# Kernel tuning notes

Measured on AMD Instinct MI355X. Metric: run time of the kernel, lower is better.

The kernel has to match this reference:

```python
import jax, jax.numpy as jnp
import numpy as np

B, S, IN = 32, 512, 19
DE, DD = 256, 128      # encoder / decoder d_model
HE, HD = 8, 4          # heads
LE, LD = 6, 2          # layers
FE, FD = 4 * DE, 4 * DD
EPS = 1e-5


def _ln(x, g, b):
    m = x.mean(-1, keepdims=True)
    v = ((x - m) ** 2).mean(-1, keepdims=True)
    return (x - m) / jnp.sqrt(v + EPS) * g + b


def _mha(x, qkv_w, qkv_b, out_w, out_b, kpad, nh):
    Bq, Sq, D = x.shape
    dh = D // nh
    qkv = x @ qkv_w.T + qkv_b
    q, k, v = jnp.split(qkv, 3, axis=-1)
    hs = lambda t: t.reshape(Bq, Sq, nh, dh).transpose(0, 2, 1, 3)  # -> [B,h,S,dh]
    q, k, v = hs(q), hs(k), hs(v)
    scores = jnp.einsum('bhqd,bhkd->bhqk', q, k) / float(np.sqrt(dh))
    scores = jnp.where(kpad[:, None, None, :], -1e9, scores)  # mask padded keys
    attn = jax.nn.softmax(scores, axis=-1)
    o = jnp.einsum('bhqk,bhkd->bhqd', attn, v).transpose(0, 2, 1, 3).reshape(Bq, Sq, D)
    return o @ out_w.T + out_b


def _block(x, p, kpad, nh):
    qkv_w, qkv_b, ow, ob, f1w, f1b, f2w, f2b, g1, b1, g2, b2 = p
    x = _ln(x + _mha(x, qkv_w, qkv_b, ow, ob, kpad, nh), g1, b1)
    h = jax.nn.relu(x @ f1w.T + f1b) @ f2w.T + f2b
    return _ln(x + h, g2, b2)


def _run(x, ps, kpad, nh, L):
    for i in range(L):
        x = _block(x, tuple(p[i] for p in ps), kpad, nh)
    return x


def _forward(event_tensor, w_in_enc, b_in_enc,
             enc_qkv_w, enc_qkv_b, enc_out_w, enc_out_b,
             enc_f1_w, enc_f1_b, enc_f2_w, enc_f2_b,
             enc_g1, enc_b1, enc_g2, enc_b2,
             mask_token, e2d_w,
             dec_qkv_w, dec_qkv_b, dec_out_w, dec_out_b,
             dec_f1_w, dec_f1_b, dec_f2_w, dec_f2_b,
             dec_g1, dec_b1, dec_g2, dec_b2,
             qh_w, qh_b, dth_w, dth_b,
             attention_mask, pred_mask):
    visible = attention_mask & (~pred_mask)
    counts = visible.sum(axis=1)                                  # [B]
    order = jnp.argsort(~visible, axis=1, stable=True)            # visible positions packed first, in order
    tok = event_tensor @ w_in_enc.T + b_in_enc                    # [B,S,DE]
    vis = jnp.take_along_axis(tok, order[:, :, None], axis=1)
    pos = jnp.arange(S)
    enc_pad = pos[None, :] >= counts[:, None]                      # True = padded slot
    vis = jnp.where(enc_pad[:, :, None], 0.0, vis)
    enc_ps = (enc_qkv_w, enc_qkv_b, enc_out_w, enc_out_b, enc_f1_w, enc_f1_b,
              enc_f2_w, enc_f2_b, enc_g1, enc_b1, enc_g2, enc_b2)
    enc_out = _run(vis, enc_ps, enc_pad, HE, LE)
    dec_vis = enc_out @ e2d_w.T                                    # [B,S,DD]
    idx = jnp.cumsum(visible.astype(jnp.int32), axis=1) - 1        # position -> packed index
    gathered = jnp.take_along_axis(dec_vis, jnp.clip(idx, 0)[:, :, None], axis=1)
    dec_in = jnp.where(visible[:, :, None], gathered, mask_token)  # mask token at masked/pad slots
    dec_ps = (dec_qkv_w, dec_qkv_b, dec_out_w, dec_out_b, dec_f1_w, dec_f1_b,
              dec_f2_w, dec_f2_b, dec_g1, dec_b1, dec_g2, dec_b2)
    dec_out = _run(dec_in, dec_ps, ~attention_mask, HD, LD)
    q = dec_out @ qh_w.T + qh_b
    dt = dec_out @ dth_w.T + dth_b
    return jnp.concatenate([q, dt], axis=-1)                       # [B,S,2]


def setup_inputs():
    key = jax.random.key(0)
    ks = iter(jax.random.split(key, 64))
    nrm = lambda shp, s=0.02: jax.random.normal(next(ks), shp, jnp.float32) * s
    d = {}
    d['event_tensor'] = jax.random.normal(next(ks), (B, S, IN), jnp.float32)
    lengths = jax.random.randint(next(ks), (B,), S // 2, S + 1)
    pos = jnp.arange(S)
    am = pos[None, :] < lengths[:, None]
    pm = (jax.random.uniform(next(ks), (B, S)) < 0.75) & am
    pm = pm.at[:, 0].set(False)  # guarantee >=1 visible token per row
    d['attention_mask'] = am
    d['pred_mask'] = pm
    d['w_in_enc'] = nrm((DE, IN)); d['b_in_enc'] = jnp.zeros((DE,), jnp.float32)
    d['enc_qkv_w'] = nrm((LE, 3 * DE, DE)); d['enc_qkv_b'] = jnp.zeros((LE, 3 * DE), jnp.float32)
    d['enc_out_w'] = nrm((LE, DE, DE));     d['enc_out_b'] = jnp.zeros((LE, DE), jnp.float32)
    d['enc_f1_w'] = nrm((LE, FE, DE));      d['enc_f1_b'] = jnp.zeros((LE, FE), jnp.float32)
    d['enc_f2_w'] = nrm((LE, DE, FE));      d['enc_f2_b'] = jnp.zeros((LE, DE), jnp.float32)
    d['enc_g1'] = jnp.ones((LE, DE), jnp.float32); d['enc_b1'] = jnp.zeros((LE, DE), jnp.float32)
    d['enc_g2'] = jnp.ones((LE, DE), jnp.float32); d['enc_b2'] = jnp.zeros((LE, DE), jnp.float32)
    d['mask_token'] = nrm((DD,))
    d['e2d_w'] = nrm((DD, DE))
    d['dec_qkv_w'] = nrm((LD, 3 * DD, DD)); d['dec_qkv_b'] = jnp.zeros((LD, 3 * DD), jnp.float32)
    d['dec_out_w'] = nrm((LD, DD, DD));     d['dec_out_b'] = jnp.zeros((LD, DD), jnp.float32)
    d['dec_f1_w'] = nrm((LD, FD, DD));      d['dec_f1_b'] = jnp.zeros((LD, FD), jnp.float32)
    d['dec_f2_w'] = nrm((LD, DD, FD));      d['dec_f2_b'] = jnp.zeros((LD, DD), jnp.float32)
    d['dec_g1'] = jnp.ones((LD, DD), jnp.float32); d['dec_b1'] = jnp.zeros((LD, DD), jnp.float32)
    d['dec_g2'] = jnp.ones((LD, DD), jnp.float32); d['dec_b2'] = jnp.zeros((LD, DD), jnp.float32)
    d['qh_w'] = nrm((1, DD));  d['qh_b'] = jnp.zeros((1,), jnp.float32)
    d['dth_w'] = nrm((1, DD)); d['dth_b'] = jnp.zeros((1,), jnp.float32)
    return d


def reference(event_tensor, attention_mask, pred_mask, w_in_enc, b_in_enc,
              enc_qkv_w, enc_qkv_b, enc_out_w, enc_out_b,
              enc_f1_w, enc_f1_b, enc_f2_w, enc_f2_b,
              enc_g1, enc_b1, enc_g2, enc_b2,
              mask_token, e2d_w,
              dec_qkv_w, dec_qkv_b, dec_out_w, dec_out_b,
              dec_f1_w, dec_f1_b, dec_f2_w, dec_f2_b,
              dec_g1, dec_b1, dec_g2, dec_b2,
              qh_w, qh_b, dth_w, dth_b):
    return _forward(event_tensor, w_in_enc, b_in_enc,
                    enc_qkv_w, enc_qkv_b, enc_out_w, enc_out_b,
                    enc_f1_w, enc_f1_b, enc_f2_w, enc_f2_b,
                    enc_g1, enc_b1, enc_g2, enc_b2,
                    mask_token, e2d_w,
                    dec_qkv_w, dec_qkv_b, dec_out_w, dec_out_b,
                    dec_f1_w, dec_f1_b, dec_f2_w, dec_f2_b,
                    dec_g1, dec_b1, dec_g2, dec_b2,
                    qh_w, qh_b, dth_w, dth_b,
                    attention_mask, pred_mask)
```

## Files before the change

kernel.cpp:

```cpp
#include <hip/hip_runtime.h>
#include <hip/hip_bf16.h>

#define B_ 32
#define S_ 512
#define IN_ 19
#define DE_ 256
#define DD_ 128
#define HE_ 8
#define HD_ 4
#define LE_ 6
#define LD_ 2
#define FE_ 1024
#define FD_ 512
#define DH_ 32

typedef __attribute__((ext_vector_type(8))) short short8;
typedef __attribute__((ext_vector_type(4))) float f32x4;

__device__ __forceinline__ short f2bf(float f) {
    union { float f; unsigned u; } x; x.f = f;
    unsigned r = x.u + 0x7fff + ((x.u >> 16) & 1);
    return (short)(r >> 16);
}
__device__ __forceinline__ float bf2f(short s) {
    union { unsigned u; float f; } x; x.u = ((unsigned)(unsigned short)s) << 16;
    return x.f;
}

#define GLL16(g, l) __builtin_amdgcn_global_load_lds( \
    (const __attribute__((address_space(1))) void*)(g), \
    (__attribute__((address_space(3))) void*)(l), 16, 0, 0)

__device__ __forceinline__ void waitvm(int n) {
    switch (n) {
    case 0: asm volatile("s_waitcnt vmcnt(0)" ::: "memory"); break;
    case 1: asm volatile("s_waitcnt vmcnt(1)" ::: "memory"); break;
    case 2: asm volatile("s_waitcnt vmcnt(2)" ::: "memory"); break;
    case 3: asm volatile("s_waitcnt vmcnt(3)" ::: "memory"); break;
    case 4: asm volatile("s_waitcnt vmcnt(4)" ::: "memory"); break;
    default: asm volatile("s_waitcnt vmcnt(5)" ::: "memory"); break;
    }
}
__device__ __forceinline__ void wait_lgkm0() {
    asm volatile("s_waitcnt lgkmcnt(0)" ::: "memory");
}

#define QSCALE 0.2550653169f

#define NCONV 9
struct ConvTab {
    const float* src[NCONV];
    short* dst[NCONV];
    int len[NCONV];
};
__global__ __launch_bounds__(S_) void conv_plan_kernel(
    ConvTab tab, int total,
    const int* __restrict__ am, const int* __restrict__ pm,
    int* __restrict__ counts, int* __restrict__ lengths, int* __restrict__ order,
    int* __restrict__ visible, int* __restrict__ idx) {
    if (blockIdx.x < B_) {
        int b = blockIdx.x, s = threadIdx.x;
        __shared__ int sc[S_];
        int a = (am[b * S_ + s] != 0);
        int v = a && (pm[b * S_ + s] == 0);
        visible[b * S_ + s] = v;
        sc[s] = v | (a << 16);
        __syncthreads();
#pragma unroll
        for (int off = 1; off < S_; off <<= 1) {
            int t = (s >= off) ? sc[s - off] : 0;
            __syncthreads();
            sc[s] += t;
            __syncthreads();
        }
        int incl = sc[s] & 0xffff;
        int tot = sc[S_ - 1];
        int total2 = tot & 0xffff;
        if (s == 0) { counts[b] = total2; lengths[b] = tot >> 16; }
        idx[b * S_ + s] = (incl > 0) ? incl - 1 : 0;
        if (v) order[b * S_ + incl - 1] = s;
        else   order[b * S_ + total2 + (s - incl)] = s;
    } else {
        int i = (blockIdx.x - B_) * S_ + threadIdx.x;
        if (i >= total) return;
        int j = i;
        for (int e = 0; e < NCONV; ++e) {
            if (j < tab.len[e]) { tab.dst[e][j] = f2bf(tab.src[e][j]); return; }
            j -= tab.len[e];
        }
    }
}

__global__ __launch_bounds__(DE_) void enc_embed_kernel(
    const float* __restrict__ ev, const float* __restrict__ w, const float* __restrict__ bias,
    const int* __restrict__ counts, const int* __restrict__ order, short* __restrict__ out) {
    int bs = blockIdx.x;
    int b = bs / S_, s = bs % S_;
    int d = threadIdx.x;
    __shared__ float e[IN_];
    bool padded = (s >= counts[b]);
    int src = order[bs];
    if (threadIdx.x < IN_)
        e[threadIdx.x] = padded ? 0.f : ev[(size_t)(b * S_ + src) * IN_ + threadIdx.x];
    __syncthreads();
    float acc = bias[d];
#pragma unroll
    for (int i = 0; i < IN_; ++i) acc += e[i] * w[d * IN_ + i];
    out[(size_t)bs * DE_ + d] = padded ? f2bf(0.f) : f2bf(acc);
}

template <int TM, int TN, bool RELU, bool QKV, int DEPTH>
__device__ __forceinline__ void gemm_body(
    const short* __restrict__ A, const short* __restrict__ Wt, const float* __restrict__ bias,
    short* __restrict__ C, int N, int K,
    short* __restrict__ qb, short* __restrict__ kb, short* __restrict__ vtb, int H, int D,
    const int* __restrict__ live) {
    constexpr int HM = TM / 2, HN = TN / 2;
    constexpr int MI = HM / 16, NI = HN / 16;
    constexpr int NCHA = TM / 16, NCH = (TM + TN) / 16;
    int bm = blockIdx.y * TM, bn = blockIdx.x * TN;
    if (live && (bm & (S_ - 1)) >= live[bm >> 9]) return;
    __shared__ short As[DEPTH][TM][32];
    __shared__ short Bs[DEPTH][TN][32];
    int t = threadIdx.x;
    int wave = t >> 6, lane = t & 63;
    int wm = (wave >> 1) * HM, wn = (wave & 1) * HN;
    int c = lane & 15, quad = lane >> 4;
    f32x4 acc[MI][NI];
#pragma unroll
    for (int i = 0; i < MI; ++i)
#pragma unroll
        for (int j = 0; j < NI; ++j) acc[i][j] = (f32x4){0.f, 0.f, 0.f, 0.f};

    int srow = lane >> 2, scol = (lane & 3) * 8;
    const int myloads = (NCH - wave + 3) >> 2;
    int nk = K >> 5;

    auto stage = [&](int buf, int kt) {
        int k0 = kt << 5;
#pragma unroll
        for (int ch0 = 0; ch0 < NCH; ch0 += 4) {
            int ch = ch0 + wave;
            if (ch < NCHA)
                GLL16(A + (size_t)(bm + ch * 16 + srow) * K + k0 + scol, &As[buf][ch * 16][0]);
            else if (ch < NCH)
                GLL16(Wt + (size_t)(bn + (ch - NCHA) * 16 + srow) * K + k0 + scol,
                      &Bs[buf][(ch - NCHA) * 16][0]);
        }
    };

#pragma unroll
    for (int i = 0; i < DEPTH - 1; ++i)
        if (i < nk) stage(i, i);

    for (int kt = 0; kt < nk; ++kt) {
        int cur = kt % DEPTH;
        int smax = (nk - 1 < kt + DEPTH - 2) ? nk - 1 : kt + DEPTH - 2;
        waitvm((smax - kt) * myloads);
        wait_lgkm0();
        __builtin_amdgcn_s_barrier();
        __builtin_amdgcn_sched_barrier(0);
        int nxt = kt + DEPTH - 1;
        if (nxt < nk) stage(nxt % DEPTH, nxt);
        short8 av[MI], bv[NI];
#pragma unroll
        for (int mi = 0; mi < MI; ++mi) av[mi] = *(const short8*)&As[cur][wm + mi * 16 + c][quad * 8];
#pragma unroll
        for (int ni = 0; ni < NI; ++ni) bv[ni] = *(const short8*)&Bs[cur][wn + ni * 16 + c][quad * 8];
#pragma unroll
        for (int mi = 0; mi < MI; ++mi)
#pragma unroll
            for (int ni = 0; ni < NI; ++ni)
                acc[mi][ni] = __builtin_amdgcn_mfma_f32_16x16x32_bf16(av[mi], bv[ni], acc[mi][ni], 0, 0, 0);
    }
#pragma unroll
    for (int mi = 0; mi < MI; ++mi)
#pragma unroll
        for (int ni = 0; ni < NI; ++ni)
#pragma unroll
            for (int r = 0; r < 4; ++r) {
                int R = bm + wm + mi * 16 + quad * 4 + r;
                int Ncol = bn + wn + ni * 16 + c;
                float v = acc[mi][ni][r] + (bias ? bias[Ncol] : 0.f);
                if (RELU) v = fmaxf(v, 0.f);
                if (!QKV) {
                    C[(size_t)R * N + Ncol] = f2bf(v);
                } else {
                    int s = R & (S_ - 1), b2 = R >> 9;
                    if (Ncol < D) {
                        int h = Ncol >> 5, d = Ncol & 31;
                        qb[(((size_t)b2 * H + h) * S_ + s) * DH_ + d] = f2bf(v * QSCALE);
                    } else if (Ncol < 2 * D) {
                        int n2 = Ncol - D, h = n2 >> 5, d = n2 & 31;
                        kb[(((size_t)b2 * H + h) * S_ + s) * DH_ + d] = f2bf(v);
                    } else {
                        int n2 = Ncol - 2 * D, h = n2 >> 5, d = n2 & 31;
                        vtb[(((size_t)b2 * H + h) * DH_ + d) * S_ + s] = f2bf(v);
                    }
                }
            }
}

template <int N, bool HEAD>
__device__ __forceinline__ void gemm_ln_body(
    const short* __restrict__ A, const short* __restrict__ Wt,
    const float* __restrict__ bias, const short* x ,
    const float* __restrict__ g, const float* __restrict__ be,
    short* out,
    const float* __restrict__ qw, const float* __restrict__ qbb,
    const float* __restrict__ dw, const float* __restrict__ dbb,
    float* __restrict__ outf,
    int K, const int* __restrict__ live) {
    constexpr int TM = 32;
    constexpr int DEPTH = 3;
    constexpr int HN = N / 2, NI = HN / 16;
    constexpr int NCHA = TM / 16, NCH = NCHA + N / 16;
    constexpr int HST = N + 8;
    constexpr int BUF = (TM + N) * 32;
    int bm = blockIdx.x * TM;
    if (live && (bm & (S_ - 1)) >= live[bm >> 9]) return;
    __shared__ short smem[DEPTH * BUF];
    int t = threadIdx.x, wave = t >> 6, lane = t & 63;
    int wm = (wave >> 1) * 16, wn = (wave & 1) * HN;
    int c = lane & 15, quad = lane >> 4;
    int srow = lane >> 2, scol = (lane & 3) * 8;
    f32x4 acc[NI];
#pragma unroll
    for (int ni = 0; ni < NI; ++ni) acc[ni] = (f32x4){0.f, 0.f, 0.f, 0.f};
    const int myloads = (NCH - wave + 3) >> 2;
    int nk = K >> 5;

    auto stage = [&](int buf, int kt) {
        short* base = smem + buf * BUF;
        int k0 = kt << 5;
#pragma unroll
        for (int ch0 = 0; ch0 < NCH; ch0 += 4) {
            int ch = ch0 + wave;
            if (ch < NCHA)
                GLL16(A + (size_t)(bm + ch * 16 + srow) * K + k0 + scol, base + ch * 16 * 32);
            else if (ch < NCH)
                GLL16(Wt + (size_t)((ch - NCHA) * 16 + srow) * K + k0 + scol,
                      base + (TM + (ch - NCHA) * 16) * 32);
        }
    };

#pragma unroll
    for (int i = 0; i < DEPTH - 1; ++i)
        if (i < nk) stage(i, i);

    for (int kt = 0; kt < nk; ++kt) {
        int cur = kt % DEPTH;
        int smax = (nk - 1 < kt + DEPTH - 2) ? nk - 1 : kt + DEPTH - 2;
        waitvm((smax - kt) * myloads);
        wait_lgkm0();
        __builtin_amdgcn_s_barrier();
        __builtin_amdgcn_sched_barrier(0);
        int nxt = kt + DEPTH - 1;
        if (nxt < nk) stage(nxt % DEPTH, nxt);
        const short* base = smem + cur * BUF;
        short8 av = *(const short8*)(base + (wm + c) * 32 + quad * 8);
        short8 bv[NI];
#pragma unroll
        for (int ni = 0; ni < NI; ++ni)
            bv[ni] = *(const short8*)(base + (TM + wn + ni * 16 + c) * 32 + quad * 8);
#pragma unroll
        for (int ni = 0; ni < NI; ++ni)
            acc[ni] = __builtin_amdgcn_mfma_f32_16x16x32_bf16(av, bv[ni], acc[ni], 0, 0, 0);
    }
    __syncthreads();

    short* Hs = smem;
#pragma unroll
    for (int ni = 0; ni < NI; ++ni) {
        int col = wn + ni * 16 + c;
        float bcol = bias[col];
#pragma unroll
        for (int r = 0; r < 4; ++r)
            Hs[(wm + quad * 4 + r) * HST + col] = f2bf(acc[ni][r] + bcol);
    }
    __syncthreads();

    constexpr int CPL = N / 8;
    int r = t >> 3, li = t & 7;
    int R = bm + r;
    int c0 = li * CPL;
    float v[CPL];
    float s = 0.f;
#pragma unroll
    for (int e8 = 0; e8 < CPL / 8; ++e8) {
        short8 xv = *(const short8*)&x[(size_t)R * N + c0 + e8 * 8];
#pragma unroll
        for (int j = 0; j < 8; ++j) {
            float vv = bf2f(xv[j]) + bf2f(Hs[r * HST + c0 + e8 * 8 + j]);
            v[e8 * 8 + j] = vv;
            s += vv;
        }
    }
    s += __shfl_xor(s, 1); s += __shfl_xor(s, 2); s += __shfl_xor(s, 4);
    float m = s / N;
    float s2 = 0.f;
#pragma unroll
    for (int e = 0; e < CPL; ++e) { float d = v[e] - m; s2 += d * d; }
    s2 += __shfl_xor(s2, 1); s2 += __shfl_xor(s2, 2); s2 += __shfl_xor(s2, 4);
    float rstd = rsqrtf(s2 / N + 1e-5f);
    if (!HEAD) {
        if (live && ((R & (S_ - 1)) >= live[R >> 9])) return;
#pragma unroll
        for (int e8 = 0; e8 < CPL / 8; ++e8) {
            short8 ov;
#pragma unroll
            for (int j = 0; j < 8; ++j) {
                int e = e8 * 8 + j;
                ov[j] = f2bf((v[e] - m) * rstd * g[c0 + e] + be[c0 + e]);
            }
            *(short8*)&out[(size_t)R * N + c0 + e8 * 8] = ov;
        }
    } else {
        float q = 0.f, dt = 0.f;
#pragma unroll
        for (int e = 0; e < CPL; ++e) {
            float o = (v[e] - m) * rstd * g[c0 + e] + be[c0 + e];
            q += o * qw[c0 + e];
            dt += o * dw[c0 + e];
        }
        q += __shfl_xor(q, 1); q += __shfl_xor(q, 2); q += __shfl_xor(q, 4);
        dt += __shfl_xor(dt, 1); dt += __shfl_xor(dt, 2); dt += __shfl_xor(dt, 4);
        if (li == 0) {
            outf[(size_t)R * 2 + 0] = q + qbb[0];
            outf[(size_t)R * 2 + 1] = dt + dbb[0];
        }
    }
}

__global__ __launch_bounds__(256) void g_qkv_e(
    const short* A, const short* Wt, const float* bias,
    short* qb, short* kb, short* vtb, const int* live) {
    gemm_body<64, 64, false, true, 4>(A, Wt, bias, nullptr, 3 * DE_, DE_, qb, kb, vtb, HE_, DE_, live);
}
__global__ __launch_bounds__(256) void g_qkv_d(
    const short* A, const short* Wt, const float* bias,
    short* qb, short* kb, short* vtb) {
    gemm_body<64, 64, false, true, 4>(A, Wt, bias, nullptr, 3 * DD_, DD_, qb, kb, vtb, HD_, DD_, nullptr);
}
__global__ __launch_bounds__(256) void g_f1_e(
    const short* A, const short* Wt, const float* bias, short* C, const int* live) {
    gemm_body<64, 64, true, false, 4>(A, Wt, bias, C, FE_, DE_, nullptr, nullptr, nullptr, 0, 0, live);
}
__global__ __launch_bounds__(256) void g_f1_d(
    const short* A, const short* Wt, const float* bias, short* C) {
    gemm_body<64, 64, true, false, 4>(A, Wt, bias, C, FD_, DD_, nullptr, nullptr, nullptr, 0, 0, nullptr);
}
__global__ __launch_bounds__(256) void g_e2d(
    const short* A, const short* Wt, short* C, const int* live) {
    gemm_body<32, 32, false, false, 4>(A, Wt, nullptr, C, DD_, DE_, nullptr, nullptr, nullptr, 0, 0, live);
}
__global__ __launch_bounds__(256) void g_outln_e(
    const short* A, const short* Wt, const float* bias, const short* x,
    const float* g, const float* be, short* out, const int* live) {
    gemm_ln_body<DE_, false>(A, Wt, bias, x, g, be, out, nullptr, nullptr, nullptr, nullptr, nullptr, DE_, live);
}
__global__ __launch_bounds__(256) void g_f2ln_e(
    const short* A, const short* Wt, const float* bias, const short* x,
    const float* g, const float* be, short* out, const int* live) {
    gemm_ln_body<DE_, false>(A, Wt, bias, x, g, be, out, nullptr, nullptr, nullptr, nullptr, nullptr, FE_, live);
}
__global__ __launch_bounds__(256) void g_outln_d(
    const short* A, const short* Wt, const float* bias, const short* x,
    const float* g, const float* be, short* out) {
    gemm_ln_body<DD_, false>(A, Wt, bias, x, g, be, out, nullptr, nullptr, nullptr, nullptr, nullptr, DD_, nullptr);
}
__global__ __launch_bounds__(256) void g_f2ln_d(
    const short* A, const short* Wt, const float* bias, const short* x,
    const float* g, const float* be, short* out) {
    gemm_ln_body<DD_, false>(A, Wt, bias, x, g, be, out, nullptr, nullptr, nullptr, nullptr, nullptr, FD_, nullptr);
}
__global__ __launch_bounds__(256) void g_headln(
    const short* A, const short* Wt, const float* bias, const short* x,
    const float* g, const float* be,
    const float* qw, const float* qbb, const float* dw, const float* dbb, float* outf) {
    gemm_ln_body<DD_, true>(A, Wt, bias, x, g, be, nullptr, qw, qbb, dw, dbb, outf, FD_, nullptr);
}

__global__ __launch_bounds__(256) void attn_flash(
    const short* __restrict__ qb, const short* __restrict__ kb, const short* __restrict__ vtb,
    const int* __restrict__ limit_arr, const int* __restrict__ qlim,
    short* __restrict__ o, int H, int D) {
    int b = blockIdx.z, h = blockIdx.y;
    if (qlim && (int)(blockIdx.x * 64) >= qlim[b]) return;
    int wave = threadIdx.x >> 6, lane = threadIdx.x & 63;
    int q0 = blockIdx.x * 64 + wave * 16;
    int c = lane & 15, quad = lane >> 4;
    size_t bh = (size_t)b * H + h;
    __shared__ short PtAll[4][16][132];
    short (*Pt)[132] = PtAll[wave];

    f32x4 zero = (f32x4){0.f, 0.f, 0.f, 0.f};
    short8 aq = *(const short8*)&qb[(bh * S_ + q0 + c) * DH_ + quad * 8];
    const short* kbase = kb + bh * S_ * DH_;
    const short* vbase = vtb + bh * DH_ * S_;

    int limit = limit_arr[b];
    int nchunks = (limit + 127) >> 7;

    float lrow[4] = {0.f, 0.f, 0.f, 0.f};
    f32x4 o0 = zero, o1 = zero;

    for (int kc = 0; kc < nchunks; ++kc) {
        f32x4 s[8];
#pragma unroll
        for (int nt = 0; nt < 8; ++nt) {
            short8 bk = *(const short8*)&kbase[(size_t)(kc * 128 + nt * 16 + c) * DH_ + quad * 8];
            s[nt] = __builtin_amdgcn_mfma_f32_16x16x32_bf16(aq, bk, zero, 0, 0, 0);
        }
#pragma unroll
        for (int nt = 0; nt < 8; ++nt) {
            bool ok = (kc * 128 + nt * 16 + c) < limit;
#pragma unroll
            for (int r = 0; r < 4; ++r) {
                float p = ok ? exp2f(s[nt][r]) : 0.f;
                s[nt][r] = p;
                lrow[r] += p;
            }
        }
#pragma unroll
        for (int nt = 0; nt < 8; ++nt)
#pragma unroll
            for (int r = 0; r < 4; ++r)
                Pt[quad * 4 + r][nt * 16 + c] = f2bf(s[nt][r]);
#pragma unroll
        for (int kk = 0; kk < 4; ++kk) {
            short8 ap = *(const short8*)&Pt[c][kk * 32 + quad * 8];
            short8 b0 = *(const short8*)&vbase[(size_t)c * S_ + kc * 128 + kk * 32 + quad * 8];
            short8 b1 = *(const short8*)&vbase[(size_t)(16 + c) * S_ + kc * 128 + kk * 32 + quad * 8];
            o0 = __builtin_amdgcn_mfma_f32_16x16x32_bf16(ap, b0, o0, 0, 0, 0);
            o1 = __builtin_amdgcn_mfma_f32_16x16x32_bf16(ap, b1, o1, 0, 0, 0);
        }
    }
#pragma unroll
    for (int r = 0; r < 4; ++r) {
        float l = lrow[r];
        l += __shfl_xor(l, 1);
        l += __shfl_xor(l, 2);
        l += __shfl_xor(l, 4);
        l += __shfl_xor(l, 8);
        float inv = 1.f / l;
        int row = quad * 4 + r;
        size_t base = (size_t)(b * S_ + q0 + row) * D + h * DH_;
        o[base + c] = f2bf(o0[r] * inv);
        o[base + 16 + c] = f2bf(o1[r] * inv);
    }
}

__global__ __launch_bounds__(DD_) void dec_embed_kernel(
    const short* __restrict__ dec_vis, const float* __restrict__ mask_token,
    const int* __restrict__ visible, const int* __restrict__ idx, short* __restrict__ out) {
    int bs = blockIdx.x, d = threadIdx.x;
    int b = bs / S_;
    short val = visible[bs] ? dec_vis[(size_t)(b * S_ + idx[bs]) * DD_ + d]
                            : f2bf(mask_token[d]);
    out[(size_t)bs * DD_ + d] = val;
}

extern "C" void kernel_launch(void* const* d_in, const int* in_sizes, int n_in,
                              void* d_out, int out_size, void* d_ws, size_t ws_size,
                              hipStream_t stream) {
    const float* ev      = (const float*)d_in[0];
    const int*  am       = (const int*)d_in[1];
    const int*  pm       = (const int*)d_in[2];
    const float* w_in    = (const float*)d_in[3];
    const float* b_in    = (const float*)d_in[4];
    const float* eqkv_w  = (const float*)d_in[5];
    const float* eqkv_b  = (const float*)d_in[6];
    const float* eout_w  = (const float*)d_in[7];
    const float* eout_b  = (const float*)d_in[8];
    const float* ef1_w   = (const float*)d_in[9];
    const float* ef1_b   = (const float*)d_in[10];
    const float* ef2_w   = (const float*)d_in[11];
    const float* ef2_b   = (const float*)d_in[12];
    const float* eg1     = (const float*)d_in[13];
    const float* eb1     = (const float*)d_in[14];
    const float* eg2     = (const float*)d_in[15];
    const float* eb2     = (const float*)d_in[16];
    const float* mask_tok= (const float*)d_in[17];
    const float* e2d_w   = (const float*)d_in[18];
    const float* dqkv_w  = (const float*)d_in[19];
    const float* dqkv_b  = (const float*)d_in[20];
    const float* dout_w  = (const float*)d_in[21];
    const float* dout_b  = (const float*)d_in[22];
    const float* df1_w   = (const float*)d_in[23];
    const float* df1_b   = (const float*)d_in[24];
    const float* df2_w   = (const float*)d_in[25];
    const float* df2_b   = (const float*)d_in[26];
    const float* dg1     = (const float*)d_in[27];
    const float* db1     = (const float*)d_in[28];
    const float* dg2     = (const float*)d_in[29];
    const float* db2     = (const float*)d_in[30];
    const float* qh_w    = (const float*)d_in[31];
    const float* qh_b    = (const float*)d_in[32];
    const float* dth_w   = (const float*)d_in[33];
    const float* dth_b   = (const float*)d_in[34];
    float* out = (float*)d_out;

    const int BS = B_ * S_;
    char* ws = (char*)d_ws;
    int* counts  = (int*)ws;
    int* lengths = counts + 32;
    int* order   = lengths + 32;
    int* visible = order + BS;
    int* idx     = visible + BS;

    short* wb = (short*)(ws + 256 * 1024);
    const int L_eqkv = LE_ * 3 * DE_ * DE_;
    const int L_eout = LE_ * DE_ * DE_;
    const int L_ef1  = LE_ * FE_ * DE_;
    const int L_ef2  = LE_ * DE_ * FE_;
    const int L_e2d  = DD_ * DE_;
    const int L_dqkv = LD_ * 3 * DD_ * DD_;
    const int L_dout = LD_ * DD_ * DD_;
    const int L_df1  = LD_ * FD_ * DD_;
    const int L_df2  = LD_ * DD_ * FD_;
    short* w_eqkv = wb;
    short* w_eout = w_eqkv + L_eqkv;
    short* w_ef1  = w_eout + L_eout;
    short* w_ef2  = w_ef1 + L_ef1;
    short* w_e2d  = w_ef2 + L_ef2;
    short* w_dqkv = w_e2d + L_e2d;
    short* w_dout = w_dqkv + L_dqkv;
    short* w_df1  = w_dout + L_dout;
    short* w_df2  = w_df1 + L_df1;
    const int convTotal = L_eqkv + L_eout + L_ef1 + L_ef2 + L_e2d + L_dqkv + L_dout + L_df1 + L_df2;

    short* bx    = (short*)(ws + 12 * 1024 * 1024);
    short* qbuf  = bx   + (size_t)BS * DE_;
    short* kbuf  = qbuf + (size_t)B_ * HE_ * S_ * DH_;
    short* vtbuf = kbuf + (size_t)B_ * HE_ * S_ * DH_;
    short* battn = vtbuf + (size_t)B_ * HE_ * S_ * DH_;
    short* bt    = battn + (size_t)BS * DE_;
    short* hid   = bt + (size_t)BS * DE_;

    ConvTab tab;
    tab.src[0] = eqkv_w; tab.dst[0] = w_eqkv; tab.len[0] = L_eqkv;
    tab.src[1] = eout_w; tab.dst[1] = w_eout; tab.len[1] = L_eout;
    tab.src[2] = ef1_w;  tab.dst[2] = w_ef1;  tab.len[2] = L_ef1;
    tab.src[3] = ef2_w;  tab.dst[3] = w_ef2;  tab.len[3] = L_ef2;
    tab.src[4] = e2d_w;  tab.dst[4] = w_e2d;  tab.len[4] = L_e2d;
    tab.src[5] = dqkv_w; tab.dst[5] = w_dqkv; tab.len[5] = L_dqkv;
    tab.src[6] = dout_w; tab.dst[6] = w_dout; tab.len[6] = L_dout;
    tab.src[7] = df1_w;  tab.dst[7] = w_df1;  tab.len[7] = L_df1;
    tab.src[8] = df2_w;  tab.dst[8] = w_df2;  tab.len[8] = L_df2;
    conv_plan_kernel<<<B_ + (convTotal + S_ - 1) / S_, S_, 0, stream>>>(
        tab, convTotal, am, pm, counts, lengths, order, visible, idx);
    enc_embed_kernel<<<BS, DE_, 0, stream>>>(ev, w_in, b_in, counts, order, bx);

    for (int l = 0; l < LE_; ++l) {
        g_qkv_e<<<dim3(3 * DE_ / 64, BS / 64), 256, 0, stream>>>(
            bx, w_eqkv + (size_t)l * 3 * DE_ * DE_, eqkv_b + (size_t)l * 3 * DE_,
            qbuf, kbuf, vtbuf, counts);
        attn_flash<<<dim3(S_ / 64, HE_, B_), 256, 0, stream>>>(
            qbuf, kbuf, vtbuf, counts, counts, battn, HE_, DE_);
        g_outln_e<<<BS / 32, 256, 0, stream>>>(
            battn, w_eout + (size_t)l * DE_ * DE_, eout_b + (size_t)l * DE_,
            bx, eg1 + (size_t)l * DE_, eb1 + (size_t)l * DE_, bx, counts);
        g_f1_e<<<dim3(FE_ / 64, BS / 64), 256, 0, stream>>>(
            bx, w_ef1 + (size_t)l * FE_ * DE_, ef1_b + (size_t)l * FE_, hid, counts);
        g_f2ln_e<<<BS / 32, 256, 0, stream>>>(
            hid, w_ef2 + (size_t)l * DE_ * FE_, ef2_b + (size_t)l * DE_,
            bx, eg2 + (size_t)l * DE_, eb2 + (size_t)l * DE_, bx, counts);
    }

    g_e2d<<<dim3(DD_ / 32, BS / 32), 256, 0, stream>>>(bx, w_e2d, bt, counts);
    dec_embed_kernel<<<BS, DD_, 0, stream>>>(bt, mask_tok, visible, idx, bx);

    for (int l = 0; l < LD_; ++l) {
        g_qkv_d<<<dim3(3 * DD_ / 64, BS / 64), 256, 0, stream>>>(
            bx, w_dqkv + (size_t)l * 3 * DD_ * DD_, dqkv_b + (size_t)l * 3 * DD_,
            qbuf, kbuf, vtbuf);
        attn_flash<<<dim3(S_ / 64, HD_, B_), 256, 0, stream>>>(
            qbuf, kbuf, vtbuf, lengths, nullptr, battn, HD_, DD_);
        g_outln_d<<<BS / 32, 256, 0, stream>>>(
            battn, w_dout + (size_t)l * DD_ * DD_, dout_b + (size_t)l * DD_,
            bx, dg1 + (size_t)l * DD_, db1 + (size_t)l * DD_, bx);
        g_f1_d<<<dim3(FD_ / 64, BS / 64), 256, 0, stream>>>(
            bx, w_df1 + (size_t)l * FD_ * DD_, df1_b + (size_t)l * FD_, hid);
        if (l < LD_ - 1) {
            g_f2ln_d<<<BS / 32, 256, 0, stream>>>(
                hid, w_df2 + (size_t)l * DD_ * FD_, df2_b + (size_t)l * DD_,
                bx, dg2 + (size_t)l * DD_, db2 + (size_t)l * DD_, bx);
        } else {
            g_headln<<<BS / 32, 256, 0, stream>>>(
                hid, w_df2 + (size_t)l * DD_ * FD_, df2_b + (size_t)l * DD_,
                bx, dg2 + (size_t)l * DD_, db2 + (size_t)l * DD_,
                qh_w, qh_b, dth_w, dth_b, out);
        }
    }
}
```

Before: 855.9 us.

## Load GEMM operands directly from global memory instead of LDS staging

Removes the multi-buffered global_load_lds staging pipeline in both GEMM bodies, so each wave reads its MFMA operand fragments straight from global memory, with K made a compile-time constant and the loop unrolled by four. The LN-fused GEMM is also repartitioned so each of the four waves covers all 32 rows and a quarter of the columns. This drops LDS traffic, barriers and waitcnt bookkeeping, but each fragment load is now a 16-byte strided global access with no cross-wave sharing, so it leans on L1/L2 caching and loses explicit latency hiding.

```diff
diff --git a/kernel.cpp b/kernel.cpp
--- a/kernel.cpp
+++ b/kernel.cpp
@@ -25,24 +25,6 @@
 __device__ __forceinline__ float bf2f(short s) {
     union { unsigned u; float f; } x; x.u = ((unsigned)(unsigned short)s) << 16;
     return x.f;
-}
-
-#define GLL16(g, l) __builtin_amdgcn_global_load_lds( \
-    (const __attribute__((address_space(1))) void*)(g), \
-    (__attribute__((address_space(3))) void*)(l), 16, 0, 0)
-
-__device__ __forceinline__ void waitvm(int n) {
-    switch (n) {
-    case 0: asm volatile("s_waitcnt vmcnt(0)" ::: "memory"); break;
-    case 1: asm volatile("s_waitcnt vmcnt(1)" ::: "memory"); break;
-    case 2: asm volatile("s_waitcnt vmcnt(2)" ::: "memory"); break;
-    case 3: asm volatile("s_waitcnt vmcnt(3)" ::: "memory"); break;
-    case 4: asm volatile("s_waitcnt vmcnt(4)" ::: "memory"); break;
-    default: asm volatile("s_waitcnt vmcnt(5)" ::: "memory"); break;
-    }
-}
-__device__ __forceinline__ void wait_lgkm0() {
-    asm volatile("s_waitcnt lgkmcnt(0)" ::: "memory");
 }
 
 #define QSCALE 0.2550653169f
@@ -109,19 +91,17 @@
     out[(size_t)bs * DE_ + d] = padded ? f2bf(0.f) : f2bf(acc);
 }
 
-template <int TM, int TN, bool RELU, bool QKV, int DEPTH>
+template <int TM, int TN, bool RELU, bool QKV, int K>
 __device__ __forceinline__ void gemm_body(
     const short* __restrict__ A, const short* __restrict__ Wt, const float* __restrict__ bias,
-    short* __restrict__ C, int N, int K,
+    short* __restrict__ C, int N,
     short* __restrict__ qb, short* __restrict__ kb, short* __restrict__ vtb, int H, int D,
     const int* __restrict__ live) {
     constexpr int HM = TM / 2, HN = TN / 2;
     constexpr int MI = HM / 16, NI = HN / 16;
-    constexpr int NCHA = TM / 16, NCH = (TM + TN) / 16;
+    constexpr int NK = K / 32;
     int bm = blockIdx.y * TM, bn = blockIdx.x * TN;
     if (live && (bm & (S_ - 1)) >= live[bm >> 9]) return;
-    __shared__ short As[DEPTH][TM][32];
-    __shared__ short Bs[DEPTH][TN][32];
     int t = threadIdx.x;
     int wave = t >> 6, lane = t & 63;
     int wm = (wave >> 1) * HM, wn = (wave & 1) * HN;
@@ -132,41 +112,18 @@
 #pragma unroll
         for (int j = 0; j < NI; ++j) acc[i][j] = (f32x4){0.f, 0.f, 0.f, 0.f};
 
-    int srow = lane >> 2, scol = (lane & 3) * 8;
-    const int myloads = (NCH - wave + 3) >> 2;
-    int nk = K >> 5;
-
-    auto stage = [&](int buf, int kt) {
-        int k0 = kt << 5;
-#pragma unroll
-        for (int ch0 = 0; ch0 < NCH; ch0 += 4) {
-            int ch = ch0 + wave;
-            if (ch < NCHA)
-                GLL16(A + (size_t)(bm + ch * 16 + srow) * K + k0 + scol, &As[buf][ch * 16][0]);
-            else if (ch < NCH)
-                GLL16(Wt + (size_t)(bn + (ch - NCHA) * 16 + srow) * K + k0 + scol,
-                      &Bs[buf][(ch - NCHA) * 16][0]);
-        }
-    };
-
-#pragma unroll
-    for (int i = 0; i < DEPTH - 1; ++i)
-        if (i < nk) stage(i, i);
-
-    for (int kt = 0; kt < nk; ++kt) {
-        int cur = kt % DEPTH;
-        int smax = (nk - 1 < kt + DEPTH - 2) ? nk - 1 : kt + DEPTH - 2;
-        waitvm((smax - kt) * myloads);
-        wait_lgkm0();
-        __builtin_amdgcn_s_barrier();
-        __builtin_amdgcn_sched_barrier(0);
-        int nxt = kt + DEPTH - 1;
-        if (nxt < nk) stage(nxt % DEPTH, nxt);
+    const short* Ab = A + (size_t)(bm + wm + c) * K + quad * 8;
+    const short* Bb = Wt + (size_t)(bn + wn + c) * K + quad * 8;
+
+#pragma unroll 4
+    for (int kt = 0; kt < NK; ++kt) {
         short8 av[MI], bv[NI];
 #pragma unroll
-        for (int mi = 0; mi < MI; ++mi) av[mi] = *(const short8*)&As[cur][wm + mi * 16 + c][quad * 8];
-#pragma unroll
-        for (int ni = 0; ni < NI; ++ni) bv[ni] = *(const short8*)&Bs[cur][wn + ni * 16 + c][quad * 8];
+        for (int mi = 0; mi < MI; ++mi)
+            av[mi] = *(const short8*)(Ab + (size_t)mi * 16 * K + kt * 32);
+#pragma unroll
+        for (int ni = 0; ni < NI; ++ni)
+            bv[ni] = *(const short8*)(Bb + (size_t)ni * 16 * K + kt * 32);
 #pragma unroll
         for (int mi = 0; mi < MI; ++mi)
 #pragma unroll
@@ -201,7 +158,7 @@
             }
 }
 
-template <int N, bool HEAD>
+template <int N, bool HEAD, int K>
 __device__ __forceinline__ void gemm_ln_body(
     const short* __restrict__ A, const short* __restrict__ Wt,
     const float* __restrict__ bias, const short* x ,
@@ -210,74 +167,53 @@
     const float* __restrict__ qw, const float* __restrict__ qbb,
     const float* __restrict__ dw, const float* __restrict__ dbb,
     float* __restrict__ outf,
-    int K, const int* __restrict__ live) {
+    const int* __restrict__ live) {
     constexpr int TM = 32;
-    constexpr int DEPTH = 3;
-    constexpr int HN = N / 2, NI = HN / 16;
-    constexpr int NCHA = TM / 16, NCH = NCHA + N / 16;
+    constexpr int MI = 2;
+    constexpr int HN = N / 4, NI = HN / 16;
+    constexpr int NK = K / 32;
     constexpr int HST = N + 8;
-    constexpr int BUF = (TM + N) * 32;
     int bm = blockIdx.x * TM;
     if (live && (bm & (S_ - 1)) >= live[bm >> 9]) return;
-    __shared__ short smem[DEPTH * BUF];
+    __shared__ short Hs[TM * HST];
     int t = threadIdx.x, wave = t >> 6, lane = t & 63;
-    int wm = (wave >> 1) * 16, wn = (wave & 1) * HN;
+    int wn = wave * HN;
     int c = lane & 15, quad = lane >> 4;
-    int srow = lane >> 2, scol = (lane & 3) * 8;
-    f32x4 acc[NI];
-#pragma unroll
-    for (int ni = 0; ni < NI; ++ni) acc[ni] = (f32x4){0.f, 0.f, 0.f, 0.f};
-    const int myloads = (NCH - wave + 3) >> 2;
-    int nk = K >> 5;
-
-    auto stage = [&](int buf, int kt) {
-        short* base = smem + buf * BUF;
-        int k0 = kt << 5;
-#pragma unroll
-        for (int ch0 = 0; ch0 < NCH; ch0 += 4) {
-            int ch = ch0 + wave;
-            if (ch < NCHA)
-                GLL16(A + (size_t)(bm + ch * 16 + srow) * K + k0 + scol, base + ch * 16 * 32);
-            else if (ch < NCH)
-                GLL16(Wt + (size_t)((ch - NCHA) * 16 + srow) * K + k0 + scol,
-                      base + (TM + (ch - NCHA) * 16) * 32);
-        }
-    };
-
-#pragma unroll
-    for (int i = 0; i < DEPTH - 1; ++i)
-        if (i < nk) stage(i, i);
-
-    for (int kt = 0; kt < nk; ++kt) {
-        int cur = kt % DEPTH;
-        int smax = (nk - 1 < kt + DEPTH - 2) ? nk - 1 : kt + DEPTH - 2;
-        waitvm((smax - kt) * myloads);
-        wait_lgkm0();
-        __builtin_amdgcn_s_barrier();
-        __builtin_amdgcn_sched_barrier(0);
-        int nxt = kt + DEPTH - 1;
-        if (nxt < nk) stage(nxt % DEPTH, nxt);
-        const short* base = smem + cur * BUF;
-        short8 av = *(const short8*)(base + (wm + c) * 32 + quad * 8);
-        short8 bv[NI];
+    f32x4 acc[MI][NI];
+#pragma unroll
+    for (int i = 0; i < MI; ++i)
+#pragma unroll
+        for (int j = 0; j < NI; ++j) acc[i][j] = (f32x4){0.f, 0.f, 0.f, 0.f};
+
+    const short* Ab = A + (size_t)(bm + c) * K + quad * 8;
+    const short* Bb = Wt + (size_t)(wn + c) * K + quad * 8;
+
+#pragma unroll 4
+    for (int kt = 0; kt < NK; ++kt) {
+        short8 av[MI], bv[NI];
+#pragma unroll
+        for (int mi = 0; mi < MI; ++mi)
+            av[mi] = *(const short8*)(Ab + (size_t)mi * 16 * K + kt * 32);
 #pragma unroll
         for (int ni = 0; ni < NI; ++ni)
-            bv[ni] = *(const short8*)(base + (TM + wn + ni * 16 + c) * 32 + quad * 8);
-#pragma unroll
-        for (int ni = 0; ni < NI; ++ni)
-            acc[ni] = __builtin_amdgcn_mfma_f32_16x16x32_bf16(av, bv[ni], acc[ni], 0, 0, 0);
-    }
-    __syncthreads();
-
-    short* Hs = smem;
-#pragma unroll
-    for (int ni = 0; ni < NI; ++ni) {
-        int col = wn + ni * 16 + c;
-        float bcol = bias[col];
-#pragma unroll
-        for (int r = 0; r < 4; ++r)
-            Hs[(wm + quad * 4 + r) * HST + col] = f2bf(acc[ni][r] + bcol);
-    }
+            bv[ni] = *(const short8*)(Bb + (size_t)ni * 16 * K + kt * 32);
+#pragma unroll
+        for (int mi = 0; mi < MI; ++mi)
+#pragma unroll
+            for (int ni = 0; ni < NI; ++ni)
+                acc[mi][ni] = __builtin_amdgcn_mfma_f32_16x16x32_bf16(av[mi], bv[ni], acc[mi][ni], 0, 0, 0);
+    }
+
+#pragma unroll
+    for (int mi = 0; mi < MI; ++mi)
+#pragma unroll
+        for (int ni = 0; ni < NI; ++ni) {
+            int col = wn + ni * 16 + c;
+            float bcol = bias[col];
+#pragma unroll
+            for (int r = 0; r < 4; ++r)
+                Hs[(mi * 16 + quad * 4 + r) * HST + col] = f2bf(acc[mi][ni][r] + bcol);
+        }
     __syncthreads();
 
     constexpr int CPL = N / 8;
@@ -335,50 +271,50 @@
 __global__ __launch_bounds__(256) void g_qkv_e(
     const short* A, const short* Wt, const float* bias,
     short* qb, short* kb, short* vtb, const int* live) {
-    gemm_body<64, 64, false, true, 4>(A, Wt, bias, nullptr, 3 * DE_, DE_, qb, kb, vtb, HE_, DE_, live);
+    gemm_body<64, 64, false, true, DE_>(A, Wt, bias, nullptr, 3 * DE_, qb, kb, vtb, HE_, DE_, live);
 }
 __global__ __launch_bounds__(256) void g_qkv_d(
     const short* A, const short* Wt, const float* bias,
     short* qb, short* kb, short* vtb) {
-    gemm_body<64, 64, false, true, 4>(A, Wt, bias, nullptr, 3 * DD_, DD_, qb, kb, vtb, HD_, DD_, nullptr);
+    gemm_body<64, 64, false, true, DD_>(A, Wt, bias, nullptr, 3 * DD_, qb, kb, vtb, HD_, DD_, nullptr);
 }
 __global__ __launch_bounds__(256) void g_f1_e(
     const short* A, const short* Wt, const float* bias, short* C, const int* live) {
-    gemm_body<64, 64, true, false, 4>(A, Wt, bias, C, FE_, DE_, nullptr, nullptr, nullptr, 0, 0, live);
+    gemm_body<64, 64, true, false, DE_>(A, Wt, bias, C, FE_, nullptr, nullptr, nullptr, 0, 0, live);
 }
 __global__ __launch_bounds__(256) void g_f1_d(
     const short* A, const short* Wt, const float* bias, short* C) {
-    gemm_body<64, 64, true, false, 4>(A, Wt, bias, C, FD_, DD_, nullptr, nullptr, nullptr, 0, 0, nullptr);
+    gemm_body<64, 64, true, false, DD_>(A, Wt, bias, C, FD_, nullptr, nullptr, nullptr, 0, 0, nullptr);
 }
 __global__ __launch_bounds__(256) void g_e2d(
     const short* A, const short* Wt, short* C, const int* live) {
-    gemm_body<32, 32, false, false, 4>(A, Wt, nullptr, C, DD_, DE_, nullptr, nullptr, nullptr, 0, 0, live);
+    gemm_body<32, 32, false, false, DE_>(A, Wt, nullptr, C, DD_, nullptr, nullptr, nullptr, 0, 0, live);
 }
 __global__ __launch_bounds__(256) void g_outln_e(
     const short* A, const short* Wt, const float* bias, const short* x,
     const float* g, const float* be, short* out, const int* live) {
-    gemm_ln_body<DE_, false>(A, Wt, bias, x, g, be, out, nullptr, nullptr, nullptr, nullptr, nullptr, DE_, live);
+    gemm_ln_body<DE_, false, DE_>(A, Wt, bias, x, g, be, out, nullptr, nullptr, nullptr, nullptr, nullptr, live);
 }
 __global__ __launch_bounds__(256) void g_f2ln_e(
     const short* A, const short* Wt, const float* bias, const short* x,
     const float* g, const float* be, short* out, const int* live) {
-    gemm_ln_body<DE_, false>(A, Wt, bias, x, g, be, out, nullptr, nullptr, nullptr, nullptr, nullptr, FE_, live);
+    gemm_ln_body<DE_, false, FE_>(A, Wt, bias, x, g, be, out, nullptr, nullptr, nullptr, nullptr, nullptr, live);
 }
 __global__ __launch_bounds__(256) void g_outln_d(
     const short* A, const short* Wt, const float* bias, const short* x,
     const float* g, const float* be, short* out) {
-    gemm_ln_body<DD_, false>(A, Wt, bias, x, g, be, out, nullptr, nullptr, nullptr, nullptr, nullptr, DD_, nullptr);
+    gemm_ln_body<DD_, false, DD_>(A, Wt, bias, x, g, be, out, nullptr, nullptr, nullptr, nullptr, nullptr, nullptr);
 }
 __global__ __launch_bounds__(256) void g_f2ln_d(
     const short* A, const short* Wt, const float* bias, const short* x,
     const float* g, const float* be, short* out) {
-    gemm_ln_body<DD_, false>(A, Wt, bias, x, g, be, out, nullptr, nullptr, nullptr, nullptr, nullptr, FD_, nullptr);
+    gemm_ln_body<DD_, false, FD_>(A, Wt, bias, x, g, be, out, nullptr, nullptr, nullptr, nullptr, nullptr, nullptr);
 }
 __global__ __launch_bounds__(256) void g_headln(
     const short* A, const short* Wt, const float* bias, const short* x,
     const float* g, const float* be,
     const float* qw, const float* qbb, const float* dw, const float* dbb, float* outf) {
-    gemm_ln_body<DD_, true>(A, Wt, bias, x, g, be, nullptr, qw, qbb, dw, dbb, outf, FD_, nullptr);
+    gemm_ln_body<DD_, true, FD_>(A, Wt, bias, x, g, be, nullptr, qw, qbb, dw, dbb, outf, nullptr);
 }
 
 __global__ __launch_bounds__(256) void attn_flash(
```

New measurement: 1.277 ms. 1.49x slower.
